# Optimization experiments

Measured on AMD Instinct MI355X. Metric: run time of the kernel, lower is better.

Reference implementation:

```python
import jax, jax.numpy as jnp
import numpy as np

B, N, D, E = 4, 8192, 8, 128
SCALE = float(1.0 / np.sqrt(E))  # torch MHA scaling, n_heads=1 -> head_dim=E


def _attn_dir(X, idx, mask, Wq, Wk, Wv, ipw, ipb, ow, ob):
    # X: [B,N,E]; idx, mask: [B,N,D]. Sequence per node = [self] + padded neighbors.
    neigh = jax.vmap(lambda x, i: x[i])(X, idx)               # [B,N,D,E] gather
    seq = jnp.concatenate([X[:, :, None, :], neigh], axis=2)  # [B,N,1+D,E]
    m = jnp.concatenate([jnp.ones(mask.shape[:2] + (1,), bool), mask.astype(bool)], axis=2)
    wq, wk, wv = jnp.split(ipw, 3, axis=0)                    # torch in_proj_weight [3E,E]
    bq, bk, bv = jnp.split(ipb, 3)
    # custom pre-projections (X @ W), then torch MHA in_proj (x @ w.T + b)
    q = (X @ Wq) @ wq.T + bq                                  # [B,N,E]; only self row queried
    k = (seq @ Wk) @ wk.T + bk                                # [B,N,1+D,E]
    v = (seq @ Wv) @ wv.T + bv                                # [B,N,1+D,E]
    scores = jnp.einsum('bne,bnse->bns', q, k) * SCALE
    scores = jnp.where(m, scores, jnp.finfo(scores.dtype).min)
    w = jax.nn.softmax(scores, axis=-1)
    ctx = jnp.einsum('bns,bnse->bne', w, v)
    return ctx @ ow.T + ob                                    # MHA out_proj


def setup_inputs():
    key = jax.random.key(0)
    ks = jax.random.split(key, 26)
    f32 = jnp.float32
    inp = {
        "X": jax.random.normal(ks[0], (B, N, E), f32),
        "in_idx": jax.random.randint(ks[1], (B, N, D), 0, N, dtype=jnp.int32),
        "out_idx": jax.random.randint(ks[2], (B, N, D), 0, N, dtype=jnp.int32),
        "in_mask": jax.random.randint(ks[3], (B, N, D), 0, 2, dtype=jnp.int32),
        "out_mask": jax.random.randint(ks[4], (B, N, D), 0, 2, dtype=jnp.int32),
    }
    i = 5
    for pfx in ("in_", "out_"):
        inp[pfx + "Wq"] = jax.random.uniform(ks[i], (E, E), f32) * 0.1; i += 1
        inp[pfx + "Wk"] = jax.random.uniform(ks[i], (E, E), f32) * 0.1; i += 1
        inp[pfx + "Wv"] = jax.random.uniform(ks[i], (E, E), f32) * 0.1; i += 1
        inp[pfx + "ipw"] = jax.random.normal(ks[i], (3 * E, E), f32) * 0.05; i += 1
        inp[pfx + "ipb"] = jax.random.normal(ks[i], (3 * E,), f32) * 0.02; i += 1
        inp[pfx + "ow"] = jax.random.normal(ks[i], (E, E), f32) * 0.05; i += 1
        inp[pfx + "ob"] = jax.random.normal(ks[i], (E,), f32) * 0.02; i += 1
    inp["lin_w"] = jax.random.normal(ks[i], (E, 2 * E), f32) * 0.05; i += 1
    inp["lin_b"] = jax.random.normal(ks[i], (E,), f32) * 0.02
    return inp


def reference(X, in_idx, out_idx, in_mask, out_mask,
              in_Wq, in_Wk, in_Wv, in_ipw, in_ipb, in_ow, in_ob,
              out_Wq, out_Wk, out_Wv, out_ipw, out_ipb, out_ow, out_ob,
              lin_w, lin_b):
    a_in = _attn_dir(X, in_idx, in_mask, in_Wq, in_Wk, in_Wv, in_ipw, in_ipb, in_ow, in_ob)
    a_out = _attn_dir(X, out_idx, out_mask, out_Wq, out_Wk, out_Wv, out_ipw, out_ipb, out_ow, out_ob)
    h = jnp.concatenate([a_in, a_out], axis=-1) @ lin_w.T + lin_b  # [B,N,E]
    return jax.nn.elu(h)
```

## Files before the change

kernel.cpp:

```cpp
#include <hip/hip_runtime.h>
#include <math.h>

#define NNODE 32768
constexpr float SCALE = 0.08838834764831845f;

typedef unsigned short u16;
typedef __bf16 bf16x8 __attribute__((ext_vector_type(8)));
typedef __bf16 bf16x2 __attribute__((ext_vector_type(2)));
typedef float f32x4 __attribute__((ext_vector_type(4)));

__device__ __forceinline__ u16 f2bf(float f) {
    unsigned u = __float_as_uint(f);
    u += 0x7fff + ((u >> 16) & 1);
    return (u16)(u >> 16);
}
__device__ __forceinline__ unsigned pack2bf(float lo, float hi) {
    return (unsigned)f2bf(lo) | ((unsigned)f2bf(hi) << 16);
}
__device__ __forceinline__ void unpack8(uint4 u, float* f) {
    f[0] = __uint_as_float(u.x << 16);  f[1] = __uint_as_float(u.x & 0xffff0000u);
    f[2] = __uint_as_float(u.y << 16);  f[3] = __uint_as_float(u.y & 0xffff0000u);
    f[4] = __uint_as_float(u.z << 16);  f[5] = __uint_as_float(u.z & 0xffff0000u);
    f[6] = __uint_as_float(u.w << 16);  f[7] = __uint_as_float(u.w & 0xffff0000u);
}
__device__ __forceinline__ float dot2bf(unsigned a, unsigned b, float c) {
#if __has_builtin(__builtin_amdgcn_fdot2_f32_bf16)
    union { unsigned u; bf16x2 v; } ua, ub;
    ua.u = a; ub.u = b;
    return __builtin_amdgcn_fdot2_f32_bf16(ua.v, ub.v, c, false);
#else
    float al = __uint_as_float(a << 16), ah = __uint_as_float(a & 0xffff0000u);
    float bl = __uint_as_float(b << 16), bh = __uint_as_float(b & 0xffff0000u);
    return fmaf(ah, bh, fmaf(al, bl, c));
#endif
}
__device__ __forceinline__ float dot8bf(uint4 a, uint4 b, float c) {
    c = dot2bf(a.x, b.x, c);
    c = dot2bf(a.y, b.y, c);
    c = dot2bf(a.z, b.z, c);
    c = dot2bf(a.w, b.w, c);
    return c;
}
__device__ __forceinline__ float dot128(const float* __restrict__ a,
                                        const float* __restrict__ b) {
    float s = 0.f;
    #pragma unroll
    for (int c = 0; c < 128; c += 4) {
        float4 x = *(const float4*)&a[c];
        float4 y = *(const float4*)&b[c];
        s = fmaf(x.x, y.x, s); s = fmaf(x.y, y.y, s);
        s = fmaf(x.z, y.z, s); s = fmaf(x.w, y.w, s);
    }
    return s;
}

__device__ __forceinline__ void gl_lds16(const void* g, void* l) {
    __builtin_amdgcn_global_load_lds(
        (const __attribute__((address_space(1))) unsigned int*)(uintptr_t)g,
        (__attribute__((address_space(3))) unsigned int*)(unsigned int)(uintptr_t)l,
        16, 0, 0);
}

__global__ __launch_bounds__(256) void wprep1(
    const float* __restrict__ ipw_in, const float* __restrict__ ipw_out,
    const float* __restrict__ Wq_in, const float* __restrict__ Wk_in,
    const float* __restrict__ Wv_in,
    const float* __restrict__ Wq_out, const float* __restrict__ Wk_out,
    const float* __restrict__ Wv_out,
    const float* __restrict__ ow_in, const float* __restrict__ ow_out,
    const float* __restrict__ lin_w,
    float* __restrict__ Af, float* __restrict__ Bmf,
    float* __restrict__ Wtf, float* __restrict__ RTf)
{
    int t = blockIdx.x * 256 + threadIdx.x;
    int i = t >> 7, j = t & 127;
    int task = blockIdx.y, dir = task & 1, kind = task >> 1;
    if (kind < 3) {
        const float* ipw = dir ? ipw_out : ipw_in;
        const float* W; const float* w; float* outp;
        if (kind == 0)      { W = dir ? Wq_out : Wq_in; w = ipw;          outp = Af;  }
        else if (kind == 1) { W = dir ? Wk_out : Wk_in; w = ipw + 16384;  outp = Bmf; }
        else                { W = dir ? Wv_out : Wv_in; w = ipw + 32768;  outp = Wtf; }
        outp[dir * 16384 + i * 128 + j] = dot128(W + i * 128, w + j * 128);
    } else {
        const float* ow = dir ? ow_out : ow_in;
        const float* lw = lin_w + i * 256 + dir * 128;
        float s = 0.f;
        #pragma unroll
        for (int e = 0; e < 128; e += 4) {
            float4 l4 = *(const float4*)&lw[e];
            s = fmaf(ow[e * 128 + j],       l4.x, s);
            s = fmaf(ow[(e + 1) * 128 + j], l4.y, s);
            s = fmaf(ow[(e + 2) * 128 + j], l4.z, s);
            s = fmaf(ow[(e + 3) * 128 + j], l4.w, s);
        }
        RTf[dir * 16384 + i * 128 + j] = s;
    }
}

__global__ __launch_bounds__(256) void wprep2(
    const float* __restrict__ Af, const float* __restrict__ Bmf,
    const float* __restrict__ Wtf, const float* __restrict__ RTf,
    const float* __restrict__ ipb_in, const float* __restrict__ ipb_out,
    const float* __restrict__ lin_w, const float* __restrict__ lin_b,
    const float* __restrict__ ob_in, const float* __restrict__ ob_out,
    u16* __restrict__ Bcat, u16* __restrict__ QfT,
    float* __restrict__ ycat, float* __restrict__ bfin)
{
    int task = blockIdx.y;
    int t = blockIdx.x * 256 + threadIdx.x;
    if (task < 2) {
        int dir = task, i = t >> 7, j = t & 127;
        float s = dot128(Af + dir * 16384 + j * 128, Bmf + dir * 16384 + i * 128);
        Bcat[(size_t)(dir * 128 + i) * 128 + j] = f2bf(s * SCALE);
    } else if (task < 4) {
        int dir = task - 2, i = t >> 7, j = t & 127;
        float s = dot128(Wtf + dir * 16384 + j * 128, RTf + dir * 16384 + i * 128);
        QfT[(size_t)i * 256 + dir * 128 + j] = f2bf(s);
    } else {
        if (t < 256) {
            int dir = t >> 7, d = t & 127;
            const float* bq = dir ? ipb_out : ipb_in;
            const float* rb = Bmf + dir * 16384 + d * 128;
            float s = 0.f;
            for (int f = 0; f < 128; ++f) s = fmaf(rb[f], bq[f], s);
            ycat[t] = s * SCALE;
        } else if (t < 384) {
            int g = t - 256;
            float s = lin_b[g];
            #pragma unroll
            for (int dir = 0; dir < 2; ++dir) {
                const float* bv = (dir ? ipb_out : ipb_in) + 256;
                const float* rt = RTf + dir * 16384 + g * 128;
                const float* ob = dir ? ob_out : ob_in;
                const float* lw = lin_w + g * 256 + dir * 128;
                for (int c = 0; c < 128; ++c)
                    s += bv[c] * rt[c] + ob[c] * lw[c];
            }
            bfin[g] = s;
        }
    }
}

template<int NT>
__global__ __launch_bounds__(256) void gemm_y(
    const float* __restrict__ X,
    const u16* __restrict__ BT,
    const float* __restrict__ bias,
    u16* __restrict__ C, u16* __restrict__ Xb)
{
    __shared__ __align__(16) u16 As[128 * 128];
    __shared__ __align__(16) u16 Bs[128 * 128];
    const int tid  = threadIdx.x;
    const int lane = tid & 63;
    const int wid  = tid >> 6;
    const int bm  = blockIdx.x * 128;
    const int wr = wid >> 1, wc = wid & 1;
    const int l15 = lane & 15, l4 = lane >> 4;

    #pragma unroll
    for (int i = 0; i < 8; ++i) {
        int c = i * 256 + tid;
        int r = c >> 4, cb = c & 15;
        const float* src = &X[(size_t)(bm + r) * 128 + cb * 8];
        float4 f0 = *(const float4*)src;
        float4 f1 = *(const float4*)(src + 4);
        uint4 pk;
        pk.x = pack2bf(f0.x, f0.y); pk.y = pack2bf(f0.z, f0.w);
        pk.z = pack2bf(f1.x, f1.y); pk.w = pack2bf(f1.z, f1.w);
        *(uint4*)&As[r * 128 + ((cb ^ (r & 7)) * 8)] = pk;
        *(uint4*)&Xb[(size_t)(bm + r) * 128 + cb * 8] = pk;
    }
    __syncthreads();
    bf16x8 a[4][4];
    #pragma unroll
    for (int ks = 0; ks < 4; ++ks)
        #pragma unroll
        for (int mr = 0; mr < 4; ++mr) {
            int r = wr * 64 + mr * 16 + l15;
            int kb = ks * 4 + l4;
            a[ks][mr] = *(const bf16x8*)((const char*)As + r * 256 + ((kb ^ (r & 7)) << 4));
        }

    #pragma unroll
    for (int nt = 0; nt < NT; ++nt) {
        int bn = nt * 128;
        __syncthreads();
        #pragma unroll
        for (int i = 0; i < 8; ++i) {
            int c = i * 256 + tid;
            int r = c >> 4, cb = c & 15;
            gl_lds16(&BT[(size_t)(bn + r) * 128 + 8 * (cb ^ (r & 7))],
                     &Bs[(size_t)(c - lane) * 8]);
        }
        __syncthreads();

        f32x4 acc[4][4] = {};
        #pragma unroll
        for (int ks = 0; ks < 4; ++ks) {
            bf16x8 bfr[4];
            #pragma unroll
            for (int nc = 0; nc < 4; ++nc) {
                int r = wc * 64 + nc * 16 + l15;
                int kb = ks * 4 + l4;
                bfr[nc] = *(const bf16x8*)((const char*)Bs + r * 256 + ((kb ^ (r & 7)) << 4));
            }
            #pragma unroll
            for (int mr = 0; mr < 4; ++mr)
                #pragma unroll
                for (int nc = 0; nc < 4; ++nc)
                    acc[mr][nc] = __builtin_amdgcn_mfma_f32_16x16x32_bf16(
                        a[ks][mr], bfr[nc], acc[mr][nc], 0, 0, 0);
        }
        #pragma unroll
        for (int nc = 0; nc < 4; ++nc) {
            int col = bn + wc * 64 + nc * 16 + l15;
            float bv = bias[col];
            #pragma unroll
            for (int mr = 0; mr < 4; ++mr)
                #pragma unroll
                for (int j = 0; j < 4; ++j) {
                    int row = bm + wr * 64 + mr * 16 + l4 * 4 + j;
                    C[(size_t)row * 256 + col] = f2bf(acc[mr][nc][j] + bv);
                }
        }
    }
}

template<int KTOT, bool ELU_F32>
__global__ __launch_bounds__(256) void gemm_mfma(
    const u16* __restrict__ A,
    const u16* __restrict__ BT,
    const float* __restrict__ bias,
    void* __restrict__ Cout, int ldc)
{
    __shared__ __align__(16) u16 As[128 * 128];
    __shared__ __align__(16) u16 Bs[128 * 128];
    const int tid  = threadIdx.x;
    const int lane = tid & 63;
    const int wid  = tid >> 6;
    const int bm = blockIdx.x * 128;
    const int bn = blockIdx.y * 128;
    const int wr = wid >> 1, wc = wid & 1;
    const int l15 = lane & 15, l4 = lane >> 4;

    f32x4 acc[4][4] = {};

    for (int k0 = 0; k0 < KTOT; k0 += 128) {
        #pragma unroll
        for (int i = 0; i < 8; ++i) {
            int c = i * 256 + tid;
            int r = c >> 4, cb = c & 15;
            int col = k0 + 8 * (cb ^ (r & 7));
            gl_lds16(&A[(size_t)(bm + r) * KTOT + col], &As[(size_t)(c - lane) * 8]);
            gl_lds16(&BT[(size_t)(bn + r) * KTOT + col], &Bs[(size_t)(c - lane) * 8]);
        }
        __syncthreads();
        #pragma unroll
        for (int ks = 0; ks < 4; ++ks) {
            bf16x8 a[4], b[4];
            #pragma unroll
            for (int mr = 0; mr < 4; ++mr) {
                int r = wr * 64 + mr * 16 + l15;
                int kb = ks * 4 + l4;
                a[mr] = *(const bf16x8*)((const char*)As + r * 256 + ((kb ^ (r & 7)) << 4));
            }
            #pragma unroll
            for (int nc = 0; nc < 4; ++nc) {
                int r = wc * 64 + nc * 16 + l15;
                int kb = ks * 4 + l4;
                b[nc] = *(const bf16x8*)((const char*)Bs + r * 256 + ((kb ^ (r & 7)) << 4));
            }
            #pragma unroll
            for (int mr = 0; mr < 4; ++mr)
                #pragma unroll
                for (int nc = 0; nc < 4; ++nc)
                    acc[mr][nc] = __builtin_amdgcn_mfma_f32_16x16x32_bf16(
                        a[mr], b[nc], acc[mr][nc], 0, 0, 0);
        }
        __syncthreads();
    }

    #pragma unroll
    for (int nc = 0; nc < 4; ++nc) {
        int col = bn + wc * 64 + nc * 16 + l15;
        float bv = bias[col];
        #pragma unroll
        for (int mr = 0; mr < 4; ++mr) {
            #pragma unroll
            for (int j = 0; j < 4; ++j) {
                int row = bm + wr * 64 + mr * 16 + l4 * 4 + j;
                float v = acc[mr][nc][j] + bv;
                if (ELU_F32) {
                    v = v > 0.f ? v : (__expf(v) - 1.f);
                    ((float*)Cout)[(size_t)row * ldc + col] = v;
                } else {
                    ((u16*)Cout)[(size_t)row * ldc + col] = f2bf(v);
                }
            }
        }
    }
}

__global__ __launch_bounds__(256) void attn_kernel(
    const u16* __restrict__ Y, const u16* __restrict__ Xb,
    const int* __restrict__ in_idx, const int* __restrict__ out_idx,
    const int* __restrict__ in_mask, const int* __restrict__ out_mask,
    u16* __restrict__ XCTX)
{
    const int tid = threadIdx.x;
    const int g   = tid >> 4;
    const int l   = tid & 15;
    const int pair = blockIdx.x & 7;
    const int dir = pair & 1, b = pair >> 1;
    const int nl = ((blockIdx.x >> 3) << 4) + g;
    const int node = (b << 13) + nl;
    const int* idx = dir == 0 ? in_idx : out_idx;
    const int* msk = dir == 0 ? in_mask : out_mask;

    const int4 i0 = *(const int4*)&idx[(size_t)node * 8];
    const int4 i1 = *(const int4*)&idx[(size_t)node * 8 + 4];
    const int4 m0 = *(const int4*)&msk[(size_t)node * 8];
    const int4 m1 = *(const int4*)&msk[(size_t)node * 8 + 4];
    const int ii[8] = { i0.x, i0.y, i0.z, i0.w, i1.x, i1.y, i1.z, i1.w };
    const int mm[8] = { m0.x, m0.y, m0.z, m0.w, m1.x, m1.y, m1.z, m1.w };

    uint4 yv = *(const uint4*)&Y[(size_t)node * 256 + dir * 128 + l * 8];
    uint4 xv[9];
    xv[0] = *(const uint4*)&Xb[(size_t)node * 128 + l * 8];
    #pragma unroll
    for (int s = 0; s < 8; ++s)
        xv[s + 1] = *(const uint4*)&Xb[(size_t)((b << 13) + ii[s]) * 128 + l * 8];

    float sc[9];
    #pragma unroll
    for (int s = 0; s < 9; ++s)
        sc[s] = dot8bf(yv, xv[s], 0.f);

    #pragma unroll
    for (int s = 0; s < 9; ++s) {
        float x = sc[s];
        x += __shfl_xor(x, 1);
        x += __shfl_xor(x, 2);
        x += __shfl_xor(x, 4);
        x += __shfl_xor(x, 8);
        sc[s] = x;
    }
    #pragma unroll
    for (int s = 1; s < 9; ++s)
        sc[s] = mm[s - 1] ? sc[s] : -1e30f;

    float m = sc[0];
    #pragma unroll
    for (int s = 1; s < 9; ++s) m = fmaxf(m, sc[s]);
    float w[9], wsum = 0.f;
    #pragma unroll
    for (int s = 0; s < 9; ++s) { w[s] = __expf(sc[s] - m); wsum += w[s]; }
    const float inv = 1.f / wsum;

    float acc[8] = {};
    #pragma unroll
    for (int s = 0; s < 9; ++s) {
        float vf[8];
        unpack8(xv[s], vf);
        #pragma unroll
        for (int j = 0; j < 8; ++j) acc[j] = fmaf(w[s], vf[j], acc[j]);
    }
    uint4 o;
    o.x = pack2bf(acc[0] * inv, acc[1] * inv);
    o.y = pack2bf(acc[2] * inv, acc[3] * inv);
    o.z = pack2bf(acc[4] * inv, acc[5] * inv);
    o.w = pack2bf(acc[6] * inv, acc[7] * inv);
    *(uint4*)&XCTX[(size_t)node * 256 + dir * 128 + l * 8] = o;
}

extern "C" void kernel_launch(void* const* d_in, const int* in_sizes, int n_in,
                              void* d_out, int out_size, void* d_ws, size_t ws_size,
                              hipStream_t stream) {
    const float* X        = (const float*)d_in[0];
    const int*   in_idx   = (const int*)d_in[1];
    const int*   out_idx  = (const int*)d_in[2];
    const int*   in_mask  = (const int*)d_in[3];
    const int*   out_mask = (const int*)d_in[4];
    const float* Wq_in  = (const float*)d_in[5];
    const float* Wk_in  = (const float*)d_in[6];
    const float* Wv_in  = (const float*)d_in[7];
    const float* ipw_in = (const float*)d_in[8];
    const float* ipb_in = (const float*)d_in[9];
    const float* ow_in  = (const float*)d_in[10];
    const float* ob_in  = (const float*)d_in[11];
    const float* Wq_out  = (const float*)d_in[12];
    const float* Wk_out  = (const float*)d_in[13];
    const float* Wv_out  = (const float*)d_in[14];
    const float* ipw_out = (const float*)d_in[15];
    const float* ipb_out = (const float*)d_in[16];
    const float* ow_out  = (const float*)d_in[17];
    const float* ob_out  = (const float*)d_in[18];
    const float* lin_w   = (const float*)d_in[19];
    const float* lin_b   = (const float*)d_in[20];

    char* wsb = (char*)d_ws;
    u16*   Xbw  = (u16*)(wsb + 0);
    u16*   Yw   = (u16*)(wsb + 8388608);
    u16*   XCTX = (u16*)(wsb + 25165824);
    u16*   Bcat = (u16*)(wsb + 41943040);
    u16*   QfT  = (u16*)(wsb + 42008576);
    float* Af   = (float*)(wsb + 42074112);
    float* Bmf  = (float*)(wsb + 42205184);
    float* Wtf  = (float*)(wsb + 42336256);
    float* RTf  = (float*)(wsb + 42467328);
    float* ycat = (float*)(wsb + 42598400);
    float* bfin = (float*)(wsb + 42599424);

    wprep1<<<dim3(64, 8), 256, 0, stream>>>(
        ipw_in, ipw_out, Wq_in, Wk_in, Wv_in, Wq_out, Wk_out, Wv_out,
        ow_in, ow_out, lin_w, Af, Bmf, Wtf, RTf);

    wprep2<<<dim3(64, 5), 256, 0, stream>>>(
        Af, Bmf, Wtf, RTf, ipb_in, ipb_out, lin_w, lin_b, ob_in, ob_out,
        Bcat, QfT, ycat, bfin);

    gemm_y<2><<<dim3(256, 1), 256, 0, stream>>>(X, Bcat, ycat, Yw, Xbw);

    attn_kernel<<<4096, 256, 0, stream>>>(
        Yw, Xbw, in_idx, out_idx, in_mask, out_mask, XCTX);

    gemm_mfma<256, true><<<dim3(256, 1), 256, 0, stream>>>(
        XCTX, QfT, bfin, (float*)d_out, 128);
}
```

Measured before the change: 66.45 us.

## Fuse neighbor attention with final projection GEMM via shared-memory context tile

Merges the attention kernel and the final output GEMM into one kernel. Each block computes both attention directions for 32 nodes, writes the bf16 context into a swizzled LDS tile, then runs MFMA against QfT with bias and ELU. This removes the global round trip of the 16 MB XCTX buffer and one kernel launch. The cost is that QfT is read from global/L2 by every block, the GEMM tile is small, and there is less parallelism per block for the gather phase.

```diff
diff --git a/kernel.cpp b/kernel.cpp
--- a/kernel.cpp
+++ b/kernel.cpp
@@ -227,151 +227,133 @@
     }
 }
 
-template<int KTOT, bool ELU_F32>
-__global__ __launch_bounds__(256) void gemm_mfma(
-    const u16* __restrict__ A,
-    const u16* __restrict__ BT,
-    const float* __restrict__ bias,
-    void* __restrict__ Cout, int ldc)
+__global__ __launch_bounds__(256) void attn_out(
+    const u16* __restrict__ Y, const u16* __restrict__ Xb,
+    const int* __restrict__ in_idx, const int* __restrict__ out_idx,
+    const int* __restrict__ in_mask, const int* __restrict__ out_mask,
+    const u16* __restrict__ QfT, const float* __restrict__ bfin,
+    float* __restrict__ Cout)
 {
-    __shared__ __align__(16) u16 As[128 * 128];
-    __shared__ __align__(16) u16 Bs[128 * 128];
+    __shared__ __align__(16) u16 XC[32 * 256];
+
     const int tid  = threadIdx.x;
     const int lane = tid & 63;
     const int wid  = tid >> 6;
-    const int bm = blockIdx.x * 128;
-    const int bn = blockIdx.y * 128;
-    const int wr = wid >> 1, wc = wid & 1;
-    const int l15 = lane & 15, l4 = lane >> 4;
-
-    f32x4 acc[4][4] = {};
-
-    for (int k0 = 0; k0 < KTOT; k0 += 128) {
-        #pragma unroll
-        for (int i = 0; i < 8; ++i) {
-            int c = i * 256 + tid;
-            int r = c >> 4, cb = c & 15;
-            int col = k0 + 8 * (cb ^ (r & 7));
-            gl_lds16(&A[(size_t)(bm + r) * KTOT + col], &As[(size_t)(c - lane) * 8]);
-            gl_lds16(&BT[(size_t)(bn + r) * KTOT + col], &Bs[(size_t)(c - lane) * 8]);
-        }
-        __syncthreads();
-        #pragma unroll
-        for (int ks = 0; ks < 4; ++ks) {
-            bf16x8 a[4], b[4];
-            #pragma unroll
-            for (int mr = 0; mr < 4; ++mr) {
-                int r = wr * 64 + mr * 16 + l15;
+    const int l15  = lane & 15, l4 = lane >> 4;
+
+    const int bid  = blockIdx.x;
+    const int b    = (bid & 7) >> 1;
+    const int s    = ((bid >> 3) << 1) + (bid & 1);
+    const int node0 = (b << 13) + s * 32;
+
+    {
+        const int g = tid >> 4, l = tid & 15;
+        #pragma unroll
+        for (int round = 0; round < 4; ++round) {
+            const int item = round * 16 + g;
+            const int r   = item & 31;
+            const int dir = item >> 5;
+            const int node = node0 + r;
+            const int* idx = dir ? out_idx : in_idx;
+            const int* msk = dir ? out_mask : in_mask;
+
+            const int4 i0 = *(const int4*)&idx[(size_t)node * 8];
+            const int4 i1 = *(const int4*)&idx[(size_t)node * 8 + 4];
+            const int4 m0 = *(const int4*)&msk[(size_t)node * 8];
+            const int4 m1 = *(const int4*)&msk[(size_t)node * 8 + 4];
+            const int ii[8] = { i0.x, i0.y, i0.z, i0.w, i1.x, i1.y, i1.z, i1.w };
+            const int mm[8] = { m0.x, m0.y, m0.z, m0.w, m1.x, m1.y, m1.z, m1.w };
+
+            uint4 yv = *(const uint4*)&Y[(size_t)node * 256 + dir * 128 + l * 8];
+            uint4 xv[9];
+            xv[0] = *(const uint4*)&Xb[(size_t)node * 128 + l * 8];
+            #pragma unroll
+            for (int t2 = 0; t2 < 8; ++t2)
+                xv[t2 + 1] = *(const uint4*)&Xb[(size_t)((b << 13) + ii[t2]) * 128 + l * 8];
+
+            float sc[9];
+            #pragma unroll
+            for (int t2 = 0; t2 < 9; ++t2)
+                sc[t2] = dot8bf(yv, xv[t2], 0.f);
+
+            #pragma unroll
+            for (int t2 = 0; t2 < 9; ++t2) {
+                float x = sc[t2];
+                x += __shfl_xor(x, 1);
+                x += __shfl_xor(x, 2);
+                x += __shfl_xor(x, 4);
+                x += __shfl_xor(x, 8);
+                sc[t2] = x;
+            }
+            #pragma unroll
+            for (int t2 = 1; t2 < 9; ++t2)
+                sc[t2] = mm[t2 - 1] ? sc[t2] : -1e30f;
+
+            float m = sc[0];
+            #pragma unroll
+            for (int t2 = 1; t2 < 9; ++t2) m = fmaxf(m, sc[t2]);
+            float w[9], wsum = 0.f;
+            #pragma unroll
+            for (int t2 = 0; t2 < 9; ++t2) { w[t2] = __expf(sc[t2] - m); wsum += w[t2]; }
+            const float inv = 1.f / wsum;
+
+            float acc[8] = {};
+            #pragma unroll
+            for (int t2 = 0; t2 < 9; ++t2) {
+                float vf[8];
+                unpack8(xv[t2], vf);
+                #pragma unroll
+                for (int j = 0; j < 8; ++j) acc[j] = fmaf(w[t2], vf[j], acc[j]);
+            }
+            uint4 o;
+            o.x = pack2bf(acc[0] * inv, acc[1] * inv);
+            o.y = pack2bf(acc[2] * inv, acc[3] * inv);
+            o.z = pack2bf(acc[4] * inv, acc[5] * inv);
+            o.w = pack2bf(acc[6] * inv, acc[7] * inv);
+            const int chunk = (dir << 4) + l;
+            *(uint4*)((char*)XC + r * 512 + ((chunk ^ (r & 7)) << 4)) = o;
+        }
+    }
+    __syncthreads();
+
+    {
+        f32x4 acc[2][2] = {};
+        #pragma unroll
+        for (int ks = 0; ks < 8; ++ks) {
+            bf16x8 a[2], bb[2];
+            #pragma unroll
+            for (int mr = 0; mr < 2; ++mr) {
+                int r = mr * 16 + l15;
                 int kb = ks * 4 + l4;
-                a[mr] = *(const bf16x8*)((const char*)As + r * 256 + ((kb ^ (r & 7)) << 4));
-            }
-            #pragma unroll
-            for (int nc = 0; nc < 4; ++nc) {
-                int r = wc * 64 + nc * 16 + l15;
-                int kb = ks * 4 + l4;
-                b[nc] = *(const bf16x8*)((const char*)Bs + r * 256 + ((kb ^ (r & 7)) << 4));
-            }
-            #pragma unroll
-            for (int mr = 0; mr < 4; ++mr)
+                a[mr] = *(const bf16x8*)((const char*)XC + r * 512 + ((kb ^ (r & 7)) << 4));
+            }
+            #pragma unroll
+            for (int nc = 0; nc < 2; ++nc) {
+                int col = wid * 32 + nc * 16 + l15;
+                bb[nc] = *(const bf16x8*)&QfT[(size_t)col * 256 + (ks * 4 + l4) * 8];
+            }
+            #pragma unroll
+            for (int mr = 0; mr < 2; ++mr)
                 #pragma unroll
-                for (int nc = 0; nc < 4; ++nc)
+                for (int nc = 0; nc < 2; ++nc)
                     acc[mr][nc] = __builtin_amdgcn_mfma_f32_16x16x32_bf16(
-                        a[mr], b[nc], acc[mr][nc], 0, 0, 0);
-        }
-        __syncthreads();
-    }
-
-    #pragma unroll
-    for (int nc = 0; nc < 4; ++nc) {
-        int col = bn + wc * 64 + nc * 16 + l15;
-        float bv = bias[col];
-        #pragma unroll
-        for (int mr = 0; mr < 4; ++mr) {
-            #pragma unroll
-            for (int j = 0; j < 4; ++j) {
-                int row = bm + wr * 64 + mr * 16 + l4 * 4 + j;
-                float v = acc[mr][nc][j] + bv;
-                if (ELU_F32) {
+                        a[mr], bb[nc], acc[mr][nc], 0, 0, 0);
+        }
+        #pragma unroll
+        for (int nc = 0; nc < 2; ++nc) {
+            int col = wid * 32 + nc * 16 + l15;
+            float bv = bfin[col];
+            #pragma unroll
+            for (int mr = 0; mr < 2; ++mr)
+                #pragma unroll
+                for (int j = 0; j < 4; ++j) {
+                    int row = mr * 16 + l4 * 4 + j;
+                    float v = acc[mr][nc][j] + bv;
                     v = v > 0.f ? v : (__expf(v) - 1.f);
-                    ((float*)Cout)[(size_t)row * ldc + col] = v;
-                } else {
-                    ((u16*)Cout)[(size_t)row * ldc + col] = f2bf(v);
+                    Cout[(size_t)(node0 + row) * 128 + col] = v;
                 }
-            }
-        }
-    }
-}
-
-__global__ __launch_bounds__(256) void attn_kernel(
-    const u16* __restrict__ Y, const u16* __restrict__ Xb,
-    const int* __restrict__ in_idx, const int* __restrict__ out_idx,
-    const int* __restrict__ in_mask, const int* __restrict__ out_mask,
-    u16* __restrict__ XCTX)
-{
-    const int tid = threadIdx.x;
-    const int g   = tid >> 4;
-    const int l   = tid & 15;
-    const int pair = blockIdx.x & 7;
-    const int dir = pair & 1, b = pair >> 1;
-    const int nl = ((blockIdx.x >> 3) << 4) + g;
-    const int node = (b << 13) + nl;
-    const int* idx = dir == 0 ? in_idx : out_idx;
-    const int* msk = dir == 0 ? in_mask : out_mask;
-
-    const int4 i0 = *(const int4*)&idx[(size_t)node * 8];
-    const int4 i1 = *(const int4*)&idx[(size_t)node * 8 + 4];
-    const int4 m0 = *(const int4*)&msk[(size_t)node * 8];
-    const int4 m1 = *(const int4*)&msk[(size_t)node * 8 + 4];
-    const int ii[8] = { i0.x, i0.y, i0.z, i0.w, i1.x, i1.y, i1.z, i1.w };
-    const int mm[8] = { m0.x, m0.y, m0.z, m0.w, m1.x, m1.y, m1.z, m1.w };
-
-    uint4 yv = *(const uint4*)&Y[(size_t)node * 256 + dir * 128 + l * 8];
-    uint4 xv[9];
-    xv[0] = *(const uint4*)&Xb[(size_t)node * 128 + l * 8];
-    #pragma unroll
-    for (int s = 0; s < 8; ++s)
-        xv[s + 1] = *(const uint4*)&Xb[(size_t)((b << 13) + ii[s]) * 128 + l * 8];
-
-    float sc[9];
-    #pragma unroll
-    for (int s = 0; s < 9; ++s)
-        sc[s] = dot8bf(yv, xv[s], 0.f);
-
-    #pragma unroll
-    for (int s = 0; s < 9; ++s) {
-        float x = sc[s];
-        x += __shfl_xor(x, 1);
-        x += __shfl_xor(x, 2);
-        x += __shfl_xor(x, 4);
-        x += __shfl_xor(x, 8);
-        sc[s] = x;
-    }
-    #pragma unroll
-    for (int s = 1; s < 9; ++s)
-        sc[s] = mm[s - 1] ? sc[s] : -1e30f;
-
-    float m = sc[0];
-    #pragma unroll
-    for (int s = 1; s < 9; ++s) m = fmaxf(m, sc[s]);
-    float w[9], wsum = 0.f;
-    #pragma unroll
-    for (int s = 0; s < 9; ++s) { w[s] = __expf(sc[s] - m); wsum += w[s]; }
-    const float inv = 1.f / wsum;
-
-    float acc[8] = {};
-    #pragma unroll
-    for (int s = 0; s < 9; ++s) {
-        float vf[8];
-        unpack8(xv[s], vf);
-        #pragma unroll
-        for (int j = 0; j < 8; ++j) acc[j] = fmaf(w[s], vf[j], acc[j]);
-    }
-    uint4 o;
-    o.x = pack2bf(acc[0] * inv, acc[1] * inv);
-    o.y = pack2bf(acc[2] * inv, acc[3] * inv);
-    o.z = pack2bf(acc[4] * inv, acc[5] * inv);
-    o.w = pack2bf(acc[6] * inv, acc[7] * inv);
-    *(uint4*)&XCTX[(size_t)node * 256 + dir * 128 + l * 8] = o;
+        }
+    }
 }
 
 extern "C" void kernel_launch(void* const* d_in, const int* in_sizes, int n_in,
@@ -402,15 +384,14 @@
     char* wsb = (char*)d_ws;
     u16*   Xbw  = (u16*)(wsb + 0);
     u16*   Yw   = (u16*)(wsb + 8388608);
-    u16*   XCTX = (u16*)(wsb + 25165824);
-    u16*   Bcat = (u16*)(wsb + 41943040);
-    u16*   QfT  = (u16*)(wsb + 42008576);
-    float* Af   = (float*)(wsb + 42074112);
-    float* Bmf  = (float*)(wsb + 42205184);
-    float* Wtf  = (float*)(wsb + 42336256);
-    float* RTf  = (float*)(wsb + 42467328);
-    float* ycat = (float*)(wsb + 42598400);
-    float* bfin = (float*)(wsb + 42599424);
+    u16*   Bcat = (u16*)(wsb + 25165824);
+    u16*   QfT  = (u16*)(wsb + 25231360);
+    float* Af   = (float*)(wsb + 25296896);
+    float* Bmf  = (float*)(wsb + 25427968);
+    float* Wtf  = (float*)(wsb + 25559040);
+    float* RTf  = (float*)(wsb + 25690112);
+    float* ycat = (float*)(wsb + 25821184);
+    float* bfin = (float*)(wsb + 25822208);
 
     wprep1<<<dim3(64, 8), 256, 0, stream>>>(
         ipw_in, ipw_out, Wq_in, Wk_in, Wv_in, Wq_out, Wk_out, Wv_out,
@@ -422,9 +403,7 @@
 
     gemm_y<2><<<dim3(256, 1), 256, 0, stream>>>(X, Bcat, ycat, Yw, Xbw);
 
-    attn_kernel<<<4096, 256, 0, stream>>>(
-        Yw, Xbw, in_idx, out_idx, in_mask, out_mask, XCTX);
-
-    gemm_mfma<256, true><<<dim3(256, 1), 256, 0, stream>>>(
-        XCTX, QfT, bfin, (float*)d_out, 128);
-}
+    attn_out<<<1024, 256, 0, stream>>>(
+        Yw, Xbw, in_idx, out_idx, in_mask, out_mask,
+        QfT, bfin, (float*)d_out);
+}
```

Measured after the change: 65.22 us (median of 2 runs). About the same (-1.9%).
